# Kernel optimization log

Measured on AMD Instinct MI355X. Metric: run time of the kernel, lower is better.

The kernel has to match this reference:

```python
import jax, jax.numpy as jnp
import numpy as np


def sparsemax(z):
    """Euclidean projection onto the simplex (Martins & Astudillo 2016).
    z: (..., L) logits -> sparse probability vectors of same shape.
    """
    L = z.shape[-1]
    z_sorted = jnp.flip(jnp.sort(z, axis=-1), axis=-1)          # descending
    cum = jnp.cumsum(z_sorted, axis=-1)
    k = jnp.arange(1, L + 1, dtype=z.dtype)                     # 1..L
    support = 1.0 + k * z_sorted > cum                          # prefix-true mask
    k_max = jnp.sum(support, axis=-1, keepdims=True).astype(z.dtype)
    # sum of z_sorted over the support == cumsum at the last supported index
    cum_at_k = jnp.sum(jnp.where(support, z_sorted, 0.0), axis=-1, keepdims=True)
    tau = (cum_at_k - 1.0) / k_max
    return jnp.maximum(z - tau, 0.0)


def setup_inputs() -> dict:
    key = jax.random.key(0)
    k1, k2 = jax.random.split(key)
    B, K, L = 64, 16, 16384
    attention_logits = jax.random.normal(k1, (B, K, L), dtype=jnp.float32)
    rationale_mask = (jax.random.uniform(k2, (B, L)) < 0.1).astype(jnp.float32)
    return {"attention_logits": attention_logits, "rationale_mask": rationale_mask}


def reference(attention_logits, rationale_mask):
    # normalize the rationale mask into a probability target q
    q = rationale_mask / jnp.clip(
        jnp.sum(rationale_mask, axis=-1, keepdims=True), 1e-12, None
    )  # (B, L)
    p = sparsemax(attention_logits)            # (B, K, L), all heads batched
    diff = p - q[:, None, :]                   # broadcast target over heads
    # per-(example, head) loss 0.5*||p - q||^2, then mean over batch and heads
    # (= mean over heads of per-head batch means, as in the torch loop)
    return 0.5 * jnp.mean(jnp.sum(diff * diff, axis=-1))
```

## Files before the change

kernel.cpp:

```cpp
#include <hip/hip_runtime.h>

#define BB 64
#define KK 16
#define LL 16384
#define CAP 2048

__global__ __launch_bounds__(256) void mask_stats_kernel(
    const float* __restrict__ mask, float* __restrict__ stats) {
  int b = blockIdx.x;
  const float* m = mask + (size_t)b * LL;
  int t = threadIdx.x;
  float s = 0.f, sq = 0.f;
#pragma unroll
  for (int j = 0; j < 16; ++j) {
    float4 v = reinterpret_cast<const float4*>(m)[j * 256 + t];
    s  += v.x + v.y + v.z + v.w;
    sq += v.x * v.x + v.y * v.y + v.z * v.z + v.w * v.w;
  }
  for (int off = 32; off; off >>= 1) {
    s  += __shfl_xor(s, off);
    sq += __shfl_xor(sq, off);
  }
  __shared__ float ls[4], lsq[4];
  int wave = t >> 6;
  if ((t & 63) == 0) { ls[wave] = s; lsq[wave] = sq; }
  __syncthreads();
  if (t == 0) {
    float S  = ls[0] + ls[1] + ls[2] + ls[3];
    float SQ = lsq[0] + lsq[1] + lsq[2] + lsq[3];
    float inv = 1.0f / fmaxf(S, 1e-12f);
    stats[2 * b]     = inv;
    stats[2 * b + 1] = SQ * inv * inv;
  }
}

__global__ __launch_bounds__(256, 4) void sparsemax_loss_kernel(
    const float* __restrict__ logits, const float* __restrict__ mask,
    const float* __restrict__ stats, float* __restrict__ out) {
  int row = blockIdx.x;
  int b = row >> 4;
  const float* z = logits + (size_t)row * LL;
  const float* m = mask + (size_t)b * LL;
  const float4* zv = reinterpret_cast<const float4*>(z);
  int t = threadIdx.x;
  int wave = t >> 6, lane = t & 63;

  __shared__ float lds_val[CAP];
  __shared__ int   lds_idx[CAP];
  __shared__ int   lds_n;
  __shared__ float lds_f[4];

  if (t == 0) lds_n = 0;

  float4 v[16];
#pragma unroll
  for (int j = 0; j < 16; ++j) v[j] = zv[j * 256 + t];

  float mx0 = -3.0e38f, mx1 = -3.0e38f, mx2 = -3.0e38f, mx3 = -3.0e38f;
#pragma unroll
  for (int j = 0; j < 4; ++j) {
    mx0 = fmaxf(mx0, fmaxf(fmaxf(v[4*j+0].x, v[4*j+0].y), fmaxf(v[4*j+0].z, v[4*j+0].w)));
    mx1 = fmaxf(mx1, fmaxf(fmaxf(v[4*j+1].x, v[4*j+1].y), fmaxf(v[4*j+1].z, v[4*j+1].w)));
    mx2 = fmaxf(mx2, fmaxf(fmaxf(v[4*j+2].x, v[4*j+2].y), fmaxf(v[4*j+2].z, v[4*j+2].w)));
    mx3 = fmaxf(mx3, fmaxf(fmaxf(v[4*j+3].x, v[4*j+3].y), fmaxf(v[4*j+3].z, v[4*j+3].w)));
  }
  float vmax = fmaxf(fmaxf(mx0, mx1), fmaxf(mx2, mx3));
  for (int off = 32; off; off >>= 1) vmax = fmaxf(vmax, __shfl_xor(vmax, off));
  if (lane == 0) lds_f[wave] = vmax;
  __syncthreads();
  float zmax = fmaxf(fmaxf(lds_f[0], lds_f[1]), fmaxf(lds_f[2], lds_f[3]));
  float thr = zmax - 1.0f;

#pragma unroll
  for (int j = 0; j < 16; ++j) {
    int base = (j * 256 + t) * 4;
    float vv[4] = {v[j].x, v[j].y, v[j].z, v[j].w};
#pragma unroll
    for (int e = 0; e < 4; ++e) {
      if (vv[e] > thr) {
        int pos = atomicAdd(&lds_n, 1);
        if (pos < CAP) { lds_val[pos] = vv[e]; lds_idx[pos] = base + e; }
      }
    }
  }
  __syncthreads();
  int n = lds_n;
  float inv_s = stats[2 * b];
  float sumq2 = stats[2 * b + 1];
  const float scale = 0.5f / (float)(BB * KK);

  if (n <= 64) {
    if (wave == 0) {
      float c = (lane < n) ? lds_val[lane] : -3.0e38f;
#pragma unroll
      for (int size = 2; size <= 64; size <<= 1) {
#pragma unroll
        for (int stride = size >> 1; stride > 0; stride >>= 1) {
          float other = __shfl_xor(c, stride);
          bool dirDesc = ((lane & size) == 0);
          bool takeMax = (dirDesc == ((lane & stride) == 0));
          float mn = fminf(c, other), mxv = fmaxf(c, other);
          c = takeMax ? mxv : mn;
        }
      }
      float cum = c;
#pragma unroll
      for (int off = 1; off < 64; off <<= 1) {
        float y = __shfl_up(cum, off);
        if (lane >= off) cum += y;
      }
      bool sup = (lane < n) && (1.0f + (float)(lane + 1) * c > cum);
      unsigned long long bal = __ballot(sup);
      int k = __popcll(bal);
      float S = sup ? c : 0.f;
      for (int off = 32; off; off >>= 1) S += __shfl_xor(S, off);
      float tau = (S - 1.0f) / (float)k;

      float a1 = 0.f, a2 = 0.f;
      if (lane < n) {
        float val = lds_val[lane];
        float p = fmaxf(val - tau, 0.f);
        if (p > 0.f) {
          float q = m[lds_idx[lane]] * inv_s;
          a1 = p * p;
          a2 = p * q;
        }
      }
      for (int off = 32; off; off >>= 1) {
        a1 += __shfl_xor(a1, off);
        a2 += __shfl_xor(a2, off);
      }
      if (lane == 0) atomicAdd(out, (a1 - 2.f * a2 + sumq2) * scale);
    }
  } else if (n <= CAP) {
    if (wave == 0) {
      int nj = (n + 63) >> 6;
      float lo = thr, hi = zmax;
      for (int it = 0; it < 30; ++it) {
        float mid = 0.5f * (lo + hi);
        float s = 0.f;
        for (int j = 0; j < nj; ++j) {
          int i = j * 64 + lane;
          float cc = (i < n) ? lds_val[i] : -3.0e38f;
          s += fmaxf(cc - mid, 0.f);
        }
        for (int off = 32; off; off >>= 1) s += __shfl_xor(s, off);
        if (s >= 1.0f) lo = mid; else hi = mid;
      }
      float S = 0.f, kc = 0.f;
      for (int j = 0; j < nj; ++j) {
        int i = j * 64 + lane;
        float cc = (i < n) ? lds_val[i] : -3.0e38f;
        if (cc > lo) { S += cc; kc += 1.f; }
      }
      for (int off = 32; off; off >>= 1) {
        S  += __shfl_xor(S, off);
        kc += __shfl_xor(kc, off);
      }
      float tau = (S - 1.0f) / kc;

      float a1 = 0.f, a2 = 0.f;
      for (int j = 0; j < nj; ++j) {
        int i = j * 64 + lane;
        if (i < n) {
          float p = fmaxf(lds_val[i] - tau, 0.f);
          if (p > 0.f) {
            float q = m[lds_idx[i]] * inv_s;
            a1 += p * p;
            a2 += p * q;
          }
        }
      }
      for (int off = 32; off; off >>= 1) {
        a1 += __shfl_xor(a1, off);
        a2 += __shfl_xor(a2, off);
      }
      if (lane == 0) atomicAdd(out, (a1 - 2.f * a2 + sumq2) * scale);
    }
  } else {
    __shared__ float red[4], red2[4];
    float lo = thr, hi = zmax;
    for (int it = 0; it < 30; ++it) {
      float mid = 0.5f * (lo + hi);
      float s = 0.f;
      for (int j = 0; j < 16; ++j) {
        float4 vv = zv[j * 256 + t];
        s += fmaxf(vv.x - mid, 0.f) + fmaxf(vv.y - mid, 0.f) +
             fmaxf(vv.z - mid, 0.f) + fmaxf(vv.w - mid, 0.f);
      }
      for (int off = 32; off; off >>= 1) s += __shfl_xor(s, off);
      __syncthreads();
      if (lane == 0) red[wave] = s;
      __syncthreads();
      float tot = red[0] + red[1] + red[2] + red[3];
      if (tot >= 1.0f) lo = mid; else hi = mid;
    }
    float S = 0.f, kc = 0.f;
    for (int j = 0; j < 16; ++j) {
      float4 vv4 = zv[j * 256 + t];
      float vv[4] = {vv4.x, vv4.y, vv4.z, vv4.w};
      for (int e = 0; e < 4; ++e)
        if (vv[e] > lo) { S += vv[e]; kc += 1.f; }
    }
    for (int off = 32; off; off >>= 1) {
      S  += __shfl_xor(S, off);
      kc += __shfl_xor(kc, off);
    }
    __syncthreads();
    if (lane == 0) { red[wave] = S; red2[wave] = kc; }
    __syncthreads();
    S  = red[0] + red[1] + red[2] + red[3];
    kc = red2[0] + red2[1] + red2[2] + red2[3];
    float tau = (S - 1.0f) / kc;

    float a1 = 0.f, a2 = 0.f;
    for (int j = 0; j < 16; ++j) {
      int base = (j * 256 + t) * 4;
      float4 vv4 = zv[j * 256 + t];
      float vv[4] = {vv4.x, vv4.y, vv4.z, vv4.w};
      for (int e = 0; e < 4; ++e) {
        float p = fmaxf(vv[e] - tau, 0.f);
        if (p > 0.f) {
          float q = m[base + e] * inv_s;
          a1 += p * p;
          a2 += p * q;
        }
      }
    }
    for (int off = 32; off; off >>= 1) {
      a1 += __shfl_xor(a1, off);
      a2 += __shfl_xor(a2, off);
    }
    __syncthreads();
    if (lane == 0) { red[wave] = a1; red2[wave] = a2; }
    __syncthreads();
    if (t == 0) {
      a1 = red[0] + red[1] + red[2] + red[3];
      a2 = red2[0] + red2[1] + red2[2] + red2[3];
      atomicAdd(out, (a1 - 2.f * a2 + sumq2) * scale);
    }
  }
}

extern "C" void kernel_launch(void* const* d_in, const int* in_sizes, int n_in,
                              void* d_out, int out_size, void* d_ws, size_t ws_size,
                              hipStream_t stream) {
  const float* logits = (const float*)d_in[0];
  const float* mask   = (const float*)d_in[1];
  float* stats = (float*)d_ws;
  float* out   = (float*)d_out;

  hipMemsetAsync(out, 0, sizeof(float), stream);
  mask_stats_kernel<<<BB, 256, 0, stream>>>(mask, stats);
  sparsemax_loss_kernel<<<BB * KK, 256, 0, stream>>>(logits, mask, stats, out);
}
```

Before: 109.9 us.

## Fuse mask stats into main kernel with last-block final reduction

```diff
diff --git a/kernel.cpp b/kernel.cpp
--- a/kernel.cpp
+++ b/kernel.cpp
@@ -4,57 +4,37 @@
 #define KK 16
 #define LL 16384
 #define CAP 2048
-
-__global__ __launch_bounds__(256) void mask_stats_kernel(
-    const float* __restrict__ mask, float* __restrict__ stats) {
-  int b = blockIdx.x;
-  const float* m = mask + (size_t)b * LL;
-  int t = threadIdx.x;
-  float s = 0.f, sq = 0.f;
-#pragma unroll
-  for (int j = 0; j < 16; ++j) {
-    float4 v = reinterpret_cast<const float4*>(m)[j * 256 + t];
-    s  += v.x + v.y + v.z + v.w;
-    sq += v.x * v.x + v.y * v.y + v.z * v.z + v.w * v.w;
-  }
-  for (int off = 32; off; off >>= 1) {
-    s  += __shfl_xor(s, off);
-    sq += __shfl_xor(sq, off);
-  }
-  __shared__ float ls[4], lsq[4];
-  int wave = t >> 6;
-  if ((t & 63) == 0) { ls[wave] = s; lsq[wave] = sq; }
-  __syncthreads();
-  if (t == 0) {
-    float S  = ls[0] + ls[1] + ls[2] + ls[3];
-    float SQ = lsq[0] + lsq[1] + lsq[2] + lsq[3];
-    float inv = 1.0f / fmaxf(S, 1e-12f);
-    stats[2 * b]     = inv;
-    stats[2 * b + 1] = SQ * inv * inv;
-  }
-}
-
-__global__ __launch_bounds__(256, 4) void sparsemax_loss_kernel(
+#define NROW (BB * KK)
+
+__device__ unsigned int g_done = 0;
+
+__global__ __launch_bounds__(256, 4) void fused_sparsemax_loss(
     const float* __restrict__ logits, const float* __restrict__ mask,
-    const float* __restrict__ stats, float* __restrict__ out) {
+    float* __restrict__ ws, float* __restrict__ out) {
   int row = blockIdx.x;
   int b = row >> 4;
+  int kseg = row & 15;
   const float* z = logits + (size_t)row * LL;
   const float* m = mask + (size_t)b * LL;
   const float4* zv = reinterpret_cast<const float4*>(z);
+  const float4* mv = reinterpret_cast<const float4*>(m);
   int t = threadIdx.x;
   int wave = t >> 6, lane = t & 63;
 
   __shared__ float lds_val[CAP];
   __shared__ int   lds_idx[CAP];
+  __shared__ float fin[4 * NROW];
   __shared__ int   lds_n;
-  __shared__ float lds_f[4];
+  __shared__ float lds_f[4], lds_s[4], lds_sq[4];
+  __shared__ float red[4], red2[4];
+  __shared__ int   lds_last;
 
   if (t == 0) lds_n = 0;
 
   float4 v[16];
 #pragma unroll
   for (int j = 0; j < 16; ++j) v[j] = zv[j * 256 + t];
+  float4 w = mv[kseg * 256 + t];
 
   float mx0 = -3.0e38f, mx1 = -3.0e38f, mx2 = -3.0e38f, mx3 = -3.0e38f;
 #pragma unroll
@@ -65,11 +45,21 @@
     mx3 = fmaxf(mx3, fmaxf(fmaxf(v[4*j+3].x, v[4*j+3].y), fmaxf(v[4*j+3].z, v[4*j+3].w)));
   }
   float vmax = fmaxf(fmaxf(mx0, mx1), fmaxf(mx2, mx3));
-  for (int off = 32; off; off >>= 1) vmax = fmaxf(vmax, __shfl_xor(vmax, off));
-  if (lane == 0) lds_f[wave] = vmax;
+  float ms  = w.x + w.y + w.z + w.w;
+  float msq = w.x * w.x + w.y * w.y + w.z * w.z + w.w * w.w;
+  for (int off = 32; off; off >>= 1) {
+    vmax = fmaxf(vmax, __shfl_xor(vmax, off));
+    ms  += __shfl_xor(ms, off);
+    msq += __shfl_xor(msq, off);
+  }
+  if (lane == 0) { lds_f[wave] = vmax; lds_s[wave] = ms; lds_sq[wave] = msq; }
   __syncthreads();
   float zmax = fmaxf(fmaxf(lds_f[0], lds_f[1]), fmaxf(lds_f[2], lds_f[3]));
   float thr = zmax - 1.0f;
+  if (t == 0) {
+    ws[2 * NROW + 2 * row]     = lds_s[0] + lds_s[1] + lds_s[2] + lds_s[3];
+    ws[2 * NROW + 2 * row + 1] = lds_sq[0] + lds_sq[1] + lds_sq[2] + lds_sq[3];
+  }
 
 #pragma unroll
   for (int j = 0; j < 16; ++j) {
@@ -85,9 +75,8 @@
   }
   __syncthreads();
   int n = lds_n;
-  float inv_s = stats[2 * b];
-  float sumq2 = stats[2 * b + 1];
-  const float scale = 0.5f / (float)(BB * KK);
+
+  float a1 = 0.f, t2 = 0.f;
 
   if (n <= 64) {
     if (wave == 0) {
@@ -116,21 +105,20 @@
       for (int off = 32; off; off >>= 1) S += __shfl_xor(S, off);
       float tau = (S - 1.0f) / (float)k;
 
-      float a1 = 0.f, a2 = 0.f;
+      float aa1 = 0.f, aa2 = 0.f;
       if (lane < n) {
         float val = lds_val[lane];
         float p = fmaxf(val - tau, 0.f);
         if (p > 0.f) {
-          float q = m[lds_idx[lane]] * inv_s;
-          a1 = p * p;
-          a2 = p * q;
+          aa1 = p * p;
+          aa2 = p * m[lds_idx[lane]];
         }
       }
       for (int off = 32; off; off >>= 1) {
-        a1 += __shfl_xor(a1, off);
-        a2 += __shfl_xor(a2, off);
-      }
-      if (lane == 0) atomicAdd(out, (a1 - 2.f * a2 + sumq2) * scale);
+        aa1 += __shfl_xor(aa1, off);
+        aa2 += __shfl_xor(aa2, off);
+      }
+      a1 = aa1; t2 = aa2;
     }
   } else if (n <= CAP) {
     if (wave == 0) {
@@ -159,26 +147,24 @@
       }
       float tau = (S - 1.0f) / kc;
 
-      float a1 = 0.f, a2 = 0.f;
+      float aa1 = 0.f, aa2 = 0.f;
       for (int j = 0; j < nj; ++j) {
         int i = j * 64 + lane;
         if (i < n) {
           float p = fmaxf(lds_val[i] - tau, 0.f);
           if (p > 0.f) {
-            float q = m[lds_idx[i]] * inv_s;
-            a1 += p * p;
-            a2 += p * q;
+            aa1 += p * p;
+            aa2 += p * m[lds_idx[i]];
           }
         }
       }
       for (int off = 32; off; off >>= 1) {
-        a1 += __shfl_xor(a1, off);
-        a2 += __shfl_xor(a2, off);
-      }
-      if (lane == 0) atomicAdd(out, (a1 - 2.f * a2 + sumq2) * scale);
+        aa1 += __shfl_xor(aa1, off);
+        aa2 += __shfl_xor(aa2, off);
+      }
+      a1 = aa1; t2 = aa2;
     }
   } else {
-    __shared__ float red[4], red2[4];
     float lo = thr, hi = zmax;
     for (int it = 0; it < 30; ++it) {
       float mid = 0.5f * (lo + hi);
@@ -213,7 +199,7 @@
     kc = red2[0] + red2[1] + red2[2] + red2[3];
     float tau = (S - 1.0f) / kc;
 
-    float a1 = 0.f, a2 = 0.f;
+    float aa1 = 0.f, aa2 = 0.f;
     for (int j = 0; j < 16; ++j) {
       int base = (j * 256 + t) * 4;
       float4 vv4 = zv[j * 256 + t];
@@ -221,23 +207,64 @@
       for (int e = 0; e < 4; ++e) {
         float p = fmaxf(vv[e] - tau, 0.f);
         if (p > 0.f) {
-          float q = m[base + e] * inv_s;
-          a1 += p * p;
-          a2 += p * q;
+          aa1 += p * p;
+          aa2 += p * m[base + e];
         }
       }
     }
     for (int off = 32; off; off >>= 1) {
-      a1 += __shfl_xor(a1, off);
-      a2 += __shfl_xor(a2, off);
-    }
-    __syncthreads();
-    if (lane == 0) { red[wave] = a1; red2[wave] = a2; }
+      aa1 += __shfl_xor(aa1, off);
+      aa2 += __shfl_xor(aa2, off);
+    }
+    __syncthreads();
+    if (lane == 0) { red[wave] = aa1; red2[wave] = aa2; }
     __syncthreads();
     if (t == 0) {
       a1 = red[0] + red[1] + red[2] + red[3];
-      a2 = red2[0] + red2[1] + red2[2] + red2[3];
-      atomicAdd(out, (a1 - 2.f * a2 + sumq2) * scale);
+      t2 = red2[0] + red2[1] + red2[2] + red2[3];
+    }
+  }
+
+  if (t == 0) {
+    ws[2 * row]     = a1;
+    ws[2 * row + 1] = t2;
+    __threadfence();
+    unsigned old = atomicAdd(&g_done, 1u);
+    int last = (old == NROW - 1);
+    lds_last = last;
+    if (last) atomicExch(&g_done, 0u);
+  }
+  __syncthreads();
+
+  if (lds_last) {
+    __threadfence();
+    const float4* wv4 = reinterpret_cast<const float4*>(ws);
+    float4* fin4 = reinterpret_cast<float4*>(fin);
+#pragma unroll
+    for (int j = 0; j < 4; ++j) fin4[j * 256 + t] = wv4[j * 256 + t];
+    __syncthreads();
+
+    float acc = 0.f;
+    if (t < 64) {
+      float S = 0.f, SQ = 0.f;
+#pragma unroll
+      for (int kk = 0; kk < 16; ++kk) {
+        S  += fin[2 * NROW + 2 * (t * 16 + kk)];
+        SQ += fin[2 * NROW + 2 * (t * 16 + kk) + 1];
+      }
+      float inv = 1.0f / fmaxf(S, 1e-12f);
+      float sumq2 = SQ * inv * inv;
+      acc = 16.0f * sumq2;
+#pragma unroll
+      for (int kk = 0; kk < 16; ++kk) {
+        float A1 = fin[2 * (t * 16 + kk)];
+        float T2 = fin[2 * (t * 16 + kk) + 1];
+        acc += A1 - 2.0f * inv * T2;
+      }
+    }
+    if (wave == 0) {
+      for (int off = 32; off; off >>= 1) acc += __shfl_xor(acc, off);
+      if (t == 0) out[0] = acc * (0.5f / (float)(BB * KK));
     }
   }
 }
@@ -247,10 +274,8 @@
                               hipStream_t stream) {
   const float* logits = (const float*)d_in[0];
   const float* mask   = (const float*)d_in[1];
-  float* stats = (float*)d_ws;
-  float* out   = (float*)d_out;
-
-  hipMemsetAsync(out, 0, sizeof(float), stream);
-  mask_stats_kernel<<<BB, 256, 0, stream>>>(mask, stats);
-  sparsemax_loss_kernel<<<BB * KK, 256, 0, stream>>>(logits, mask, stats, out);
+  float* ws  = (float*)d_ws;
+  float* out = (float*)d_out;
+
+  fused_sparsemax_loss<<<NROW, 256, 0, stream>>>(logits, mask, ws, out);
 }
```

Result: slower. 124.4 us (+13.2%).

## Replace atomic output accumulation with per-row partials and a combine kernel

Applied to the files above, without the earlier changes.

```diff
diff --git a/kernel.cpp b/kernel.cpp
--- a/kernel.cpp
+++ b/kernel.cpp
@@ -4,6 +4,7 @@
 #define KK 16
 #define LL 16384
 #define CAP 2048
+#define NROW (BB * KK)
 
 __global__ __launch_bounds__(256) void mask_stats_kernel(
     const float* __restrict__ mask, float* __restrict__ stats) {
@@ -36,7 +37,7 @@
 
 __global__ __launch_bounds__(256, 4) void sparsemax_loss_kernel(
     const float* __restrict__ logits, const float* __restrict__ mask,
-    const float* __restrict__ stats, float* __restrict__ out) {
+    float* __restrict__ ws) {
   int row = blockIdx.x;
   int b = row >> 4;
   const float* z = logits + (size_t)row * LL;
@@ -85,9 +86,6 @@
   }
   __syncthreads();
   int n = lds_n;
-  float inv_s = stats[2 * b];
-  float sumq2 = stats[2 * b + 1];
-  const float scale = 0.5f / (float)(BB * KK);
 
   if (n <= 64) {
     if (wave == 0) {
@@ -121,16 +119,15 @@
         float val = lds_val[lane];
         float p = fmaxf(val - tau, 0.f);
         if (p > 0.f) {
-          float q = m[lds_idx[lane]] * inv_s;
           a1 = p * p;
-          a2 = p * q;
+          a2 = p * m[lds_idx[lane]];
         }
       }
       for (int off = 32; off; off >>= 1) {
         a1 += __shfl_xor(a1, off);
         a2 += __shfl_xor(a2, off);
       }
-      if (lane == 0) atomicAdd(out, (a1 - 2.f * a2 + sumq2) * scale);
+      if (lane == 0) { ws[2 * row] = a1; ws[2 * row + 1] = a2; }
     }
   } else if (n <= CAP) {
     if (wave == 0) {
@@ -165,9 +162,8 @@
         if (i < n) {
           float p = fmaxf(lds_val[i] - tau, 0.f);
           if (p > 0.f) {
-            float q = m[lds_idx[i]] * inv_s;
             a1 += p * p;
-            a2 += p * q;
+            a2 += p * m[lds_idx[i]];
           }
         }
       }
@@ -175,7 +171,7 @@
         a1 += __shfl_xor(a1, off);
         a2 += __shfl_xor(a2, off);
       }
-      if (lane == 0) atomicAdd(out, (a1 - 2.f * a2 + sumq2) * scale);
+      if (lane == 0) { ws[2 * row] = a1; ws[2 * row + 1] = a2; }
     }
   } else {
     __shared__ float red[4], red2[4];
@@ -221,9 +217,8 @@
       for (int e = 0; e < 4; ++e) {
         float p = fmaxf(vv[e] - tau, 0.f);
         if (p > 0.f) {
-          float q = m[base + e] * inv_s;
           a1 += p * p;
-          a2 += p * q;
+          a2 += p * m[base + e];
         }
       }
     }
@@ -237,9 +232,27 @@
     if (t == 0) {
       a1 = red[0] + red[1] + red[2] + red[3];
       a2 = red2[0] + red2[1] + red2[2] + red2[3];
-      atomicAdd(out, (a1 - 2.f * a2 + sumq2) * scale);
-    }
-  }
+      ws[2 * row] = a1;
+      ws[2 * row + 1] = a2;
+    }
+  }
+}
+
+__global__ __launch_bounds__(64) void combine_kernel(
+    const float* __restrict__ ws, const float* __restrict__ stats,
+    float* __restrict__ out) {
+  int t = threadIdx.x;
+  float inv   = stats[2 * t];
+  float sumq2 = stats[2 * t + 1];
+  float acc = 16.0f * sumq2;
+#pragma unroll
+  for (int kk = 0; kk < 16; ++kk) {
+    float A1 = ws[2 * (t * 16 + kk)];
+    float T2 = ws[2 * (t * 16 + kk) + 1];
+    acc += A1 - 2.0f * inv * T2;
+  }
+  for (int off = 32; off; off >>= 1) acc += __shfl_xor(acc, off);
+  if (t == 0) out[0] = acc * (0.5f / (float)(BB * KK));
 }
 
 extern "C" void kernel_launch(void* const* d_in, const int* in_sizes, int n_in,
@@ -247,10 +260,11 @@
                               hipStream_t stream) {
   const float* logits = (const float*)d_in[0];
   const float* mask   = (const float*)d_in[1];
-  float* stats = (float*)d_ws;
+  float* ws    = (float*)d_ws;
+  float* stats = (float*)d_ws + 2 * NROW;
   float* out   = (float*)d_out;
 
-  hipMemsetAsync(out, 0, sizeof(float), stream);
   mask_stats_kernel<<<BB, 256, 0, stream>>>(mask, stats);
-  sparsemax_loss_kernel<<<BB * KK, 256, 0, stream>>>(logits, mask, stats, out);
-}
+  sparsemax_loss_kernel<<<NROW, 256, 0, stream>>>(logits, mask, ws);
+  combine_kernel<<<1, 64, 0, stream>>>(ws, stats, out);
+}
```

After: 110.9 us. No clear change (+0.9%).
